# Kernel optimization log

Hardware: AMD Instinct MI355X
Metric: run time of the kernel (lower is better)

The kernel has to match this reference:

```python
import jax, jax.numpy as jnp
import numpy as np
from jax import lax

EPS = 1e-5

def binarize(x):
    # sign() forward, straight-through (identity) backward, like BinarizeConv2d's .data trick
    return x + lax.stop_gradient(jnp.sign(x) - x)

def conv_nchw(x, w, stride, pad):
    return lax.conv_general_dilated(
        x, w, window_strides=(stride, stride), padding=((pad, pad), (pad, pad)),
        dimension_numbers=('NCHW', 'OIHW', 'NCHW'))

def batchnorm_train(x, gamma, beta):
    # training-mode BN: per-channel batch mean / biased variance over (N,H,W)
    mean = jnp.mean(x, axis=(0, 2, 3), keepdims=True)
    var = jnp.mean((x - mean) ** 2, axis=(0, 2, 3), keepdims=True)
    xhat = (x - mean) * lax.rsqrt(var + EPS)
    return xhat * gamma[None, :, None, None] + beta[None, :, None, None]

def hardtanh(x):
    return jnp.clip(x, -1.0, 1.0)

def setup_inputs() -> dict:
    key = jax.random.key(0)
    ks = jax.random.split(key, 7)
    N, Cin, Cout, H, W = 32, 64, 64, 128, 128
    x = jax.random.normal(ks[0], (N, Cin, H, W), dtype=jnp.float32)
    w1 = jax.random.normal(ks[1], (Cout, Cin, 3, 3), dtype=jnp.float32) * 0.05
    w2 = jax.random.normal(ks[2], (Cout, Cout, 3, 3), dtype=jnp.float32) * 0.05
    g1 = jnp.ones((Cout,), dtype=jnp.float32)
    b1 = jnp.zeros((Cout,), dtype=jnp.float32)
    g2 = jnp.ones((Cout,), dtype=jnp.float32)
    b2 = jnp.zeros((Cout,), dtype=jnp.float32)
    return {"x": x, "w1": w1, "g1": g1, "b1": b1, "w2": w2, "g2": g2, "b2": b2}

def reference(x, w1, g1, b1, w2, g2, b2):
    # conv1: binarized input (C=64 != 3) and binarized weights
    out = conv_nchw(binarize(x), binarize(w1), stride=1, pad=1)
    out = hardtanh(batchnorm_train(out, g1, b1))
    # conv2: 3x3, stride 1 (stride==1 branch)
    out = conv_nchw(binarize(out), binarize(w2), stride=1, pad=1)
    out = batchnorm_train(out, g2, b2)
    # identity shortcut (stride==1 and in_planes==planes)
    out = out + x
    return hardtanh(out)
```

## Files before the change

kernel.cpp:

```cpp
#include <hip/hip_runtime.h>
#include <stdint.h>

typedef unsigned long long u64;
typedef unsigned int u32;

#define Nn 32
#define Cc 64
#define Hh 128
#define Ww 128
#define HPAD 130
#define WPAD 130
#define NHW_TOT (Nn*Hh*Ww)
#define NBIN 8

__device__ __forceinline__ float2 compute_ab(const u64* __restrict__ sum, const u64* __restrict__ sq,
        const float* __restrict__ g, const float* __restrict__ bet, int c) {
    long long Sv = 0, Qv = 0;
    #pragma unroll
    for (int b = 0; b < NBIN; ++b) {
        Sv += (long long)sum[b * 64 + c];
        Qv += (long long)sq[b * 64 + c];
    }
    double mean = (double)Sv / (double)NHW_TOT;
    double var = (double)Qv / (double)NHW_TOT - mean * mean;
    double invstd = 1.0 / sqrt(var + 1e-5);
    double a = (double)g[c] * invstd;
    double b_ = (double)bet[c] - a * mean;
    return make_float2((float)a, (float)b_);
}

__global__ __launch_bounds__(256) void pack_x4_kernel(const float* __restrict__ x,
                                                      u64* __restrict__ xpad) {
    int t = blockIdx.x * 256 + threadIdx.x;
    int P = t * 4;
    int row = P >> 7, w0 = P & 127;
    int n = row >> 7, h = row & 127;
    const float4* xp4 = (const float4*)(x + ((size_t)n * Cc * Hh + h) * Ww + w0);
    u32 lo0 = 0, lo1 = 0, lo2 = 0, lo3 = 0, hi0 = 0, hi1 = 0, hi2 = 0, hi3 = 0;
    #pragma unroll 8
    for (int c = 0; c < 32; ++c) {
        float4 v = xp4[c * (Hh * Ww / 4)];
        lo0 |= (__float_as_uint(v.x) >> 31) << c;
        lo1 |= (__float_as_uint(v.y) >> 31) << c;
        lo2 |= (__float_as_uint(v.z) >> 31) << c;
        lo3 |= (__float_as_uint(v.w) >> 31) << c;
    }
    #pragma unroll 8
    for (int c = 32; c < 64; ++c) {
        float4 v = xp4[c * (Hh * Ww / 4)];
        hi0 |= (__float_as_uint(v.x) >> 31) << (c - 32);
        hi1 |= (__float_as_uint(v.y) >> 31) << (c - 32);
        hi2 |= (__float_as_uint(v.z) >> 31) << (c - 32);
        hi3 |= (__float_as_uint(v.w) >> 31) << (c - 32);
    }
    u64* dst = xpad + ((size_t)n * HPAD + h + 1) * WPAD + w0 + 1;
    dst[0] = ((u64)hi0 << 32) | lo0;
    dst[1] = ((u64)hi1 << 32) | lo1;
    dst[2] = ((u64)hi2 << 32) | lo2;
    dst[3] = ((u64)hi3 << 32) | lo3;
}

__global__ __launch_bounds__(576) void pack_w_kernel(
        const float* __restrict__ w1, const float* __restrict__ w2,
        u64* __restrict__ w1b, u64* __restrict__ w2b) {
    int t = threadIdx.x;
    const float* src = blockIdx.x ? w2 : w1;
    u64* db = blockIdx.x ? w2b : w1b;
    int co = t / 9, tap = t - co * 9;
    const float* p = src + (size_t)co * 576 + tap;
    u32 lo = 0, hi = 0;
    #pragma unroll
    for (int ci = 0; ci < 32; ++ci)
        lo |= (__float_as_uint(p[ci * 9]) >> 31) << ci;
    #pragma unroll
    for (int ci = 32; ci < 64; ++ci)
        hi |= (__float_as_uint(p[ci * 9]) >> 31) << (ci - 32);
    db[t] = ((u64)hi << 32) | lo;
}

__device__ __forceinline__ void conv4(const u64* __restrict__ L0, const u64* __restrict__ L1,
                                      const u64* __restrict__ L2, int w,
                                      const u64 W[9], int corrMid, int v[4]) {
    u64 a[6], b[6], c[6];
    #pragma unroll
    for (int j = 0; j < 6; ++j) { a[j] = L0[w + j]; b[j] = L1[w + j]; c[j] = L2[w + j]; }
    #pragma unroll
    for (int px = 0; px < 4; ++px) {
        int p0 = __popcll(a[px] ^ W[0]) + __popcll(a[px + 1] ^ W[1]) + __popcll(a[px + 2] ^ W[2]);
        int p1 = __popcll(b[px] ^ W[3]) + __popcll(b[px + 1] ^ W[4]) + __popcll(b[px + 2] ^ W[5]);
        int p2 = __popcll(c[px] ^ W[6]) + __popcll(c[px + 1] ^ W[7]) + __popcll(c[px + 2] ^ W[8]);
        v[px] = 576 - 2 * (p0 + p1 + p2) - corrMid;
    }
}

struct LaneCtx {
    u64 W[9];
    int corrMid, corrW0, corrW127;
    int n, h;
};

__device__ __forceinline__ void lane_setup(LaneCtx& C, const u64* __restrict__ wb,
                                           int lane, int blk, int wv) {
    C.n = blk >> 5;
    int hb = (blk & 31) << 2;
    C.h = hb + wv;
    #pragma unroll
    for (int t = 0; t < 9; ++t) C.W[t] = wb[lane * 9 + t];
    int wc[9];
    #pragma unroll
    for (int t = 0; t < 9; ++t) wc[t] = 64 - 2 * __popcll(C.W[t]);
    int tT = wc[0] + wc[1] + wc[2], tB = wc[6] + wc[7] + wc[8];
    int tL = wc[0] + wc[3] + wc[6], tR = wc[2] + wc[5] + wc[8];
    bool fT = (C.h == 0), fB = (C.h == 127);
    C.corrMid  = (fT ? tT : 0) + (fB ? tB : 0);
    C.corrW0   = tL - (fT ? wc[0] : 0) - (fB ? wc[6] : 0);
    C.corrW127 = tR - (fT ? wc[2] : 0) - (fB ? wc[8] : 0);
}

template<bool SPILL>
__global__ __launch_bounds__(256) void conv_statsT(const u64* __restrict__ inpad,
        const u64* __restrict__ wb, u64* __restrict__ gsum, u64* __restrict__ gsq,
        short* __restrict__ v16) {
    __shared__ u64 win[6 * 130];
    int tid = threadIdx.x;
    int lane = tid & 63;
    int wv = __builtin_amdgcn_readfirstlane(tid >> 6);
    int blk = blockIdx.x;
    int n = blk >> 5, hb = (blk & 31) << 2;
    const u64* src = inpad + ((size_t)n * HPAD + hb) * WPAD;
    for (int i = tid; i < 780; i += 256) win[i] = src[i];
    LaneCtx C;
    lane_setup(C, wb, lane, blk, wv);
    __syncthreads();
    const u64* L0 = &win[wv * 130];
    const u64* L1 = L0 + 130;
    const u64* L2 = L0 + 260;
    short* vrow = SPILL ? (v16 + ((size_t)(C.n * Hh + C.h) * Ww) * 64 + lane) : nullptr;
    int s = 0, q = 0;
    for (int w = 0; w < 128; w += 4) {
        int v[4];
        conv4(L0, L1, L2, w, C.W, C.corrMid, v);
        if (w == 0)   v[0] -= C.corrW0;
        if (w == 124) v[3] -= C.corrW127;
        #pragma unroll
        for (int px = 0; px < 4; ++px) {
            s += v[px];
            q += __mul24(v[px], v[px]);
            if (SPILL) vrow[(size_t)(w + px) * 64] = (short)v[px];
        }
    }
    __syncthreads();
    int* r32 = (int*)win;
    r32[wv * 64 + lane] = s;
    r32[256 + wv * 64 + lane] = q;
    __syncthreads();
    if (wv == 0) {
        int S = r32[lane] + r32[64 + lane] + r32[128 + lane] + r32[192 + lane];
        int Q = r32[256 + lane] + r32[320 + lane] + r32[384 + lane] + r32[448 + lane];
        int bin = blk & (NBIN - 1);
        atomicAdd(&gsum[bin * 64 + lane], (u64)(long long)S);
        atomicAdd(&gsq[bin * 64 + lane], (u64)(long long)Q);
    }
}

__global__ __launch_bounds__(256) void signpack_v(const short* __restrict__ v16,
        const u64* __restrict__ sum, const u64* __restrict__ sq,
        const float* __restrict__ g, const float* __restrict__ bet,
        u64* __restrict__ ypad) {
    int tid = threadIdx.x;
    int lane = tid & 63;
    int wv = tid >> 6;
    int grow = blockIdx.x * 4 + wv;
    int n = grow >> 7, h = grow & 127;
    float2 ab = compute_ab(sum, sq, g, bet, lane);
    const short* vr = v16 + (size_t)grow * (Ww * 64) + lane;
    u64* drow = ypad + ((size_t)n * HPAD + h + 1) * WPAD + 1;
    for (int base = 0; base < 128; base += 64) {
        u64 myw = 0;
        #pragma unroll 8
        for (int px = 0; px < 64; ++px) {
            float tv = fmaf((float)vr[(size_t)(base + px) * 64], ab.x, ab.y);
            u64 bal = __ballot(tv < 0.0f);
            if (lane == px) myw = bal;
        }
        drow[base + lane] = myw;
    }
}

__global__ __launch_bounds__(256) void signpack_rc(const u64* __restrict__ inpad,
        const u64* __restrict__ wb, const u64* __restrict__ sum, const u64* __restrict__ sq,
        const float* __restrict__ g, const float* __restrict__ bet,
        u64* __restrict__ outpad) {
    __shared__ u64 win[6 * 130];
    int tid = threadIdx.x;
    int lane = tid & 63;
    int wv = __builtin_amdgcn_readfirstlane(tid >> 6);
    int blk = blockIdx.x;
    int n = blk >> 5, hb = (blk & 31) << 2;
    const u64* src = inpad + ((size_t)n * HPAD + hb) * WPAD;
    for (int i = tid; i < 780; i += 256) win[i] = src[i];
    LaneCtx C;
    lane_setup(C, wb, lane, blk, wv);
    float2 ab = compute_ab(sum, sq, g, bet, lane);
    __syncthreads();
    const u64* L0 = &win[wv * 130];
    const u64* L1 = L0 + 130;
    const u64* L2 = L0 + 260;
    u64* drow = outpad + ((size_t)C.n * HPAD + C.h + 1) * WPAD + 1;
    for (int w = 0; w < 128; w += 4) {
        int v[4];
        conv4(L0, L1, L2, w, C.W, C.corrMid, v);
        if (w == 0)   v[0] -= C.corrW0;
        if (w == 124) v[3] -= C.corrW127;
        u64 wd[4];
        #pragma unroll
        for (int px = 0; px < 4; ++px) {
            float t = fmaf((float)v[px], ab.x, ab.y);
            wd[px] = __ballot(t < 0.0f);
        }
        if (lane == 0) {
            drow[w] = wd[0]; drow[w + 1] = wd[1]; drow[w + 2] = wd[2]; drow[w + 3] = wd[3];
        }
    }
}

__global__ __launch_bounds__(256) void final4_kernel(const u64* __restrict__ inpad,
        const u64* __restrict__ wb, const u64* __restrict__ sum, const u64* __restrict__ sq,
        const float* __restrict__ g, const float* __restrict__ bet,
        const float* __restrict__ x, float* __restrict__ out) {
    __shared__ u64 win[6 * 130];
    __shared__ float tile[4][64 * 33];
    int tid = threadIdx.x;
    int lane = tid & 63;
    int wv = __builtin_amdgcn_readfirstlane(tid >> 6);
    int blk = blockIdx.x;
    int n = blk >> 5, hb = (blk & 31) << 2;
    const u64* src = inpad + ((size_t)n * HPAD + hb) * WPAD;
    for (int i = tid; i < 780; i += 256) win[i] = src[i];
    LaneCtx C;
    lane_setup(C, wb, lane, blk, wv);
    float2 ab = compute_ab(sum, sq, g, bet, lane);
    float aa = ab.x, bb = ab.y;
    __syncthreads();
    const u64* L0 = &win[wv * 130];
    const u64* L1 = L0 + 130;
    const u64* L2 = L0 + 260;
    float* T = tile[wv];
    int p4 = lane & 7;
    int cosub = lane >> 3;
    size_t base_nch = ((size_t)C.n * Cc * Hh + C.h) * Ww;
    for (int w = 0; w < 128; w += 4) {
        int v[4];
        conv4(L0, L1, L2, w, C.W, C.corrMid, v);
        if (w == 0)   v[0] -= C.corrW0;
        if (w == 124) v[3] -= C.corrW127;
        #pragma unroll
        for (int px = 0; px < 4; ++px) {
            float t = fmaf((float)v[px], aa, bb);
            T[lane * 33 + ((w + px) & 31)] = t;
        }
        if ((w & 31) == 28) {
            int w0 = w & ~31;
            #pragma unroll 8
            for (int st = 0; st < 8; ++st) {
                int co = st * 8 + cosub;
                size_t idx = base_nch + (size_t)co * (Hh * Ww) + w0 + p4 * 4;
                float4 xv = *(const float4*)(x + idx);
                float y0 = T[co * 33 + p4 * 4 + 0] + xv.x;
                float y1 = T[co * 33 + p4 * 4 + 1] + xv.y;
                float y2 = T[co * 33 + p4 * 4 + 2] + xv.z;
                float y3 = T[co * 33 + p4 * 4 + 3] + xv.w;
                float4 yv;
                yv.x = fminf(1.0f, fmaxf(-1.0f, y0));
                yv.y = fminf(1.0f, fmaxf(-1.0f, y1));
                yv.z = fminf(1.0f, fmaxf(-1.0f, y2));
                yv.w = fminf(1.0f, fmaxf(-1.0f, y3));
                *(float4*)(out + idx) = yv;
            }
        }
    }
}

extern "C" void kernel_launch(void* const* d_in, const int* in_sizes, int n_in,
                              void* d_out, int out_size, void* d_ws, size_t ws_size,
                              hipStream_t stream) {
    const float* x  = (const float*)d_in[0];
    const float* w1 = (const float*)d_in[1];
    const float* g1 = (const float*)d_in[2];
    const float* b1 = (const float*)d_in[3];
    const float* w2 = (const float*)d_in[4];
    const float* g2 = (const float*)d_in[5];
    const float* b2 = (const float*)d_in[6];
    float* out = (float*)d_out;
    char* ws = (char*)d_ws;

    constexpr size_t SZ_PAD   = (size_t)Nn * HPAD * WPAD * sizeof(u64);
    constexpr size_t OFF_YPAD = SZ_PAD;
    constexpr size_t OFF_STAT = 2 * SZ_PAD;
    constexpr size_t SZ_STAT  = (size_t)NBIN * 64 * 8;
    constexpr size_t OFF_W1B  = OFF_STAT + 4 * SZ_STAT;
    constexpr size_t OFF_W2B  = OFF_W1B + 576 * 8;
    constexpr size_t OFF_V16  = OFF_W2B + 576 * 8;
    constexpr size_t SZ_V16   = (size_t)Nn * Hh * Ww * 64 * 2;
    constexpr size_t WS_SMALL = OFF_V16;
    constexpr size_t WS_FULL  = OFF_V16 + SZ_V16;

    if (ws_size < WS_SMALL) return;
    bool spill = (ws_size >= WS_FULL);

    u64* xpad = (u64*)(ws);
    u64* ypad = (u64*)(ws + OFF_YPAD);
    u64* gsum1 = (u64*)(ws + OFF_STAT);
    u64* gsq1  = (u64*)(ws + OFF_STAT + SZ_STAT);
    u64* gsum2 = (u64*)(ws + OFF_STAT + 2 * SZ_STAT);
    u64* gsq2  = (u64*)(ws + OFF_STAT + 3 * SZ_STAT);
    u64* w1b  = (u64*)(ws + OFF_W1B);
    u64* w2b  = (u64*)(ws + OFF_W2B);
    short* v16 = (short*)(ws + OFF_V16);

    hipMemsetAsync(ws, 0, 2 * SZ_PAD + 4 * SZ_STAT, stream);

    pack_x4_kernel<<<512, 256, 0, stream>>>(x, xpad);
    pack_w_kernel<<<2, 576, 0, stream>>>(w1, w2, w1b, w2b);
    if (spill) {
        conv_statsT<true><<<1024, 256, 0, stream>>>(xpad, w1b, gsum1, gsq1, v16);
        signpack_v<<<1024, 256, 0, stream>>>(v16, gsum1, gsq1, g1, b1, ypad);
    } else {
        conv_statsT<false><<<1024, 256, 0, stream>>>(xpad, w1b, gsum1, gsq1, nullptr);
        signpack_rc<<<1024, 256, 0, stream>>>(xpad, w1b, gsum1, gsq1, g1, b1, ypad);
    }
    conv_statsT<false><<<1024, 256, 0, stream>>>(ypad, w2b, gsum2, gsq2, nullptr);
    final4_kernel<<<1024, 256, 0, stream>>>(ypad, w2b, gsum2, gsq2, g2, b2, x, out);
}
```

Before: 228.1 us.

## Split conv blocks into half-row tiles with more blocks and smaller LDS

The conv-stats and final kernels are retiled from one 256-thread block per four full rows to 128-thread blocks covering two rows and half the width. This gives a 4096-block grid with a smaller LDS window. The final kernel now stages raw conv values as shorts in LDS, computes the BN affine per channel from a shared table, and applies it while reading back. The stat bins double to 16 to spread out atomic contention, and signpack_v now gives each wave half a row. The goal is more parallelism and occupancy, at the cost of redundant halo loads and more per-block setup such as loading weights.

```diff
diff --git a/kernel.cpp b/kernel.cpp
--- a/kernel.cpp
+++ b/kernel.cpp
@@ -11,7 +11,7 @@
 #define HPAD 130
 #define WPAD 130
 #define NHW_TOT (Nn*Hh*Ww)
-#define NBIN 8
+#define NBIN 16
 
 __device__ __forceinline__ float2 compute_ab(const u64* __restrict__ sum, const u64* __restrict__ sq,
         const float* __restrict__ g, const float* __restrict__ bet, int c) {
@@ -96,14 +96,10 @@
 struct LaneCtx {
     u64 W[9];
     int corrMid, corrW0, corrW127;
-    int n, h;
 };
 
 __device__ __forceinline__ void lane_setup(LaneCtx& C, const u64* __restrict__ wb,
-                                           int lane, int blk, int wv) {
-    C.n = blk >> 5;
-    int hb = (blk & 31) << 2;
-    C.h = hb + wv;
+                                           int lane, int h) {
     #pragma unroll
     for (int t = 0; t < 9; ++t) C.W[t] = wb[lane * 9 + t];
     int wc[9];
@@ -111,37 +107,44 @@
     for (int t = 0; t < 9; ++t) wc[t] = 64 - 2 * __popcll(C.W[t]);
     int tT = wc[0] + wc[1] + wc[2], tB = wc[6] + wc[7] + wc[8];
     int tL = wc[0] + wc[3] + wc[6], tR = wc[2] + wc[5] + wc[8];
-    bool fT = (C.h == 0), fB = (C.h == 127);
+    bool fT = (h == 0), fB = (h == 127);
     C.corrMid  = (fT ? tT : 0) + (fB ? tB : 0);
     C.corrW0   = tL - (fT ? wc[0] : 0) - (fB ? wc[6] : 0);
     C.corrW127 = tR - (fT ? wc[2] : 0) - (fB ? wc[8] : 0);
 }
 
 template<bool SPILL>
-__global__ __launch_bounds__(256) void conv_statsT(const u64* __restrict__ inpad,
+__global__ __launch_bounds__(128) void conv_statsT(const u64* __restrict__ inpad,
         const u64* __restrict__ wb, u64* __restrict__ gsum, u64* __restrict__ gsq,
         short* __restrict__ v16) {
-    __shared__ u64 win[6 * 130];
+    __shared__ u64 win[4 * 68];
+    __shared__ int r32[256];
     int tid = threadIdx.x;
     int lane = tid & 63;
     int wv = __builtin_amdgcn_readfirstlane(tid >> 6);
     int blk = blockIdx.x;
-    int n = blk >> 5, hb = (blk & 31) << 2;
-    const u64* src = inpad + ((size_t)n * HPAD + hb) * WPAD;
-    for (int i = tid; i < 780; i += 256) win[i] = src[i];
+    int half = blk & 1;
+    int hp = (blk >> 1) & 63;
+    int n = blk >> 7;
+    int h = hp * 2 + wv;
+    const u64* src = inpad + ((size_t)n * HPAD + hp * 2) * WPAD + half * 64;
+    for (int i = tid; i < 264; i += 128) {
+        int r = i / 66, c = i - r * 66;
+        win[r * 68 + c] = src[(size_t)r * WPAD + c];
+    }
     LaneCtx C;
-    lane_setup(C, wb, lane, blk, wv);
-    __syncthreads();
-    const u64* L0 = &win[wv * 130];
-    const u64* L1 = L0 + 130;
-    const u64* L2 = L0 + 260;
-    short* vrow = SPILL ? (v16 + ((size_t)(C.n * Hh + C.h) * Ww) * 64 + lane) : nullptr;
+    lane_setup(C, wb, lane, h);
+    __syncthreads();
+    const u64* L0 = &win[wv * 68];
+    const u64* L1 = L0 + 68;
+    const u64* L2 = L0 + 136;
+    short* vrow = SPILL ? (v16 + (((size_t)(n * Hh + h) * Ww) + half * 64) * 64 + lane) : nullptr;
     int s = 0, q = 0;
-    for (int w = 0; w < 128; w += 4) {
+    for (int w = 0; w < 64; w += 4) {
         int v[4];
         conv4(L0, L1, L2, w, C.W, C.corrMid, v);
-        if (w == 0)   v[0] -= C.corrW0;
-        if (w == 124) v[3] -= C.corrW127;
+        if (half == 0 && w == 0)  v[0] -= C.corrW0;
+        if (half == 1 && w == 60) v[3] -= C.corrW127;
         #pragma unroll
         for (int px = 0; px < 4; ++px) {
             s += v[px];
@@ -150,13 +153,12 @@
         }
     }
     __syncthreads();
-    int* r32 = (int*)win;
     r32[wv * 64 + lane] = s;
-    r32[256 + wv * 64 + lane] = q;
+    r32[128 + wv * 64 + lane] = q;
     __syncthreads();
     if (wv == 0) {
-        int S = r32[lane] + r32[64 + lane] + r32[128 + lane] + r32[192 + lane];
-        int Q = r32[256 + lane] + r32[320 + lane] + r32[384 + lane] + r32[448 + lane];
+        int S = r32[lane] + r32[64 + lane];
+        int Q = r32[128 + lane] + r32[192 + lane];
         int bin = blk & (NBIN - 1);
         atomicAdd(&gsum[bin * 64 + lane], (u64)(long long)S);
         atomicAdd(&gsq[bin * 64 + lane], (u64)(long long)Q);
@@ -170,21 +172,20 @@
     int tid = threadIdx.x;
     int lane = tid & 63;
     int wv = tid >> 6;
-    int grow = blockIdx.x * 4 + wv;
+    int grow = blockIdx.x * 2 + (wv >> 1);
+    int base = (wv & 1) * 64;
     int n = grow >> 7, h = grow & 127;
     float2 ab = compute_ab(sum, sq, g, bet, lane);
-    const short* vr = v16 + (size_t)grow * (Ww * 64) + lane;
+    const short* vr = v16 + ((size_t)grow * Ww + base) * 64;
     u64* drow = ypad + ((size_t)n * HPAD + h + 1) * WPAD + 1;
-    for (int base = 0; base < 128; base += 64) {
-        u64 myw = 0;
-        #pragma unroll 8
-        for (int px = 0; px < 64; ++px) {
-            float tv = fmaf((float)vr[(size_t)(base + px) * 64], ab.x, ab.y);
-            u64 bal = __ballot(tv < 0.0f);
-            if (lane == px) myw = bal;
-        }
-        drow[base + lane] = myw;
-    }
+    u64 myw = 0;
+    #pragma unroll 8
+    for (int px = 0; px < 64; ++px) {
+        float tv = fmaf((float)vr[(size_t)px * 64 + lane], ab.x, ab.y);
+        u64 bal = __ballot(tv < 0.0f);
+        if (lane == px) myw = bal;
+    }
+    drow[base + lane] = myw;
 }
 
 __global__ __launch_bounds__(256) void signpack_rc(const u64* __restrict__ inpad,
@@ -197,16 +198,17 @@
     int wv = __builtin_amdgcn_readfirstlane(tid >> 6);
     int blk = blockIdx.x;
     int n = blk >> 5, hb = (blk & 31) << 2;
+    int h = hb + wv;
     const u64* src = inpad + ((size_t)n * HPAD + hb) * WPAD;
     for (int i = tid; i < 780; i += 256) win[i] = src[i];
     LaneCtx C;
-    lane_setup(C, wb, lane, blk, wv);
+    lane_setup(C, wb, lane, h);
     float2 ab = compute_ab(sum, sq, g, bet, lane);
     __syncthreads();
     const u64* L0 = &win[wv * 130];
     const u64* L1 = L0 + 130;
     const u64* L2 = L0 + 260;
-    u64* drow = outpad + ((size_t)C.n * HPAD + C.h + 1) * WPAD + 1;
+    u64* drow = outpad + ((size_t)n * HPAD + h + 1) * WPAD + 1;
     for (int w = 0; w < 128; w += 4) {
         int v[4];
         conv4(L0, L1, L2, w, C.W, C.corrMid, v);
@@ -224,57 +226,59 @@
     }
 }
 
-__global__ __launch_bounds__(256) void final4_kernel(const u64* __restrict__ inpad,
+__global__ __launch_bounds__(128) void final5_kernel(const u64* __restrict__ inpad,
         const u64* __restrict__ wb, const u64* __restrict__ sum, const u64* __restrict__ sq,
         const float* __restrict__ g, const float* __restrict__ bet,
         const float* __restrict__ x, float* __restrict__ out) {
-    __shared__ u64 win[6 * 130];
-    __shared__ float tile[4][64 * 33];
+    __shared__ u64 win[4 * 68];
+    __shared__ short T[2][64 * 36];
+    __shared__ float2 absh[64];
     int tid = threadIdx.x;
     int lane = tid & 63;
     int wv = __builtin_amdgcn_readfirstlane(tid >> 6);
     int blk = blockIdx.x;
-    int n = blk >> 5, hb = (blk & 31) << 2;
-    const u64* src = inpad + ((size_t)n * HPAD + hb) * WPAD;
-    for (int i = tid; i < 780; i += 256) win[i] = src[i];
+    int half = blk & 1;
+    int hp = (blk >> 1) & 63;
+    int n = blk >> 7;
+    int h = hp * 2 + wv;
+    const u64* src = inpad + ((size_t)n * HPAD + hp * 2) * WPAD + half * 64;
+    for (int i = tid; i < 264; i += 128) {
+        int r = i / 66, c = i - r * 66;
+        win[r * 68 + c] = src[(size_t)r * WPAD + c];
+    }
     LaneCtx C;
-    lane_setup(C, wb, lane, blk, wv);
-    float2 ab = compute_ab(sum, sq, g, bet, lane);
-    float aa = ab.x, bb = ab.y;
-    __syncthreads();
-    const u64* L0 = &win[wv * 130];
-    const u64* L1 = L0 + 130;
-    const u64* L2 = L0 + 260;
-    float* T = tile[wv];
+    lane_setup(C, wb, lane, h);
+    if (tid < 64) absh[tid] = compute_ab(sum, sq, g, bet, tid);
+    __syncthreads();
+    const u64* L0 = &win[wv * 68];
+    const u64* L1 = L0 + 68;
+    const u64* L2 = L0 + 136;
+    short* Tw = T[wv];
     int p4 = lane & 7;
     int cosub = lane >> 3;
-    size_t base_nch = ((size_t)C.n * Cc * Hh + C.h) * Ww;
-    for (int w = 0; w < 128; w += 4) {
+    size_t base_nch = ((size_t)n * Cc * Hh + h) * Ww;
+    for (int w = 0; w < 64; w += 4) {
         int v[4];
         conv4(L0, L1, L2, w, C.W, C.corrMid, v);
-        if (w == 0)   v[0] -= C.corrW0;
-        if (w == 124) v[3] -= C.corrW127;
-        #pragma unroll
-        for (int px = 0; px < 4; ++px) {
-            float t = fmaf((float)v[px], aa, bb);
-            T[lane * 33 + ((w + px) & 31)] = t;
-        }
+        if (half == 0 && w == 0)  v[0] -= C.corrW0;
+        if (half == 1 && w == 60) v[3] -= C.corrW127;
+        short4 sv;
+        sv.x = (short)v[0]; sv.y = (short)v[1]; sv.z = (short)v[2]; sv.w = (short)v[3];
+        *(short4*)&Tw[lane * 36 + (w & 31)] = sv;
         if ((w & 31) == 28) {
-            int w0 = w & ~31;
+            int w0g = half * 64 + (w & ~31);
             #pragma unroll 8
             for (int st = 0; st < 8; ++st) {
                 int co = st * 8 + cosub;
-                size_t idx = base_nch + (size_t)co * (Hh * Ww) + w0 + p4 * 4;
+                short4 tv = *(const short4*)&Tw[co * 36 + p4 * 4];
+                float2 cab = absh[co];
+                size_t idx = base_nch + (size_t)co * (Hh * Ww) + w0g + p4 * 4;
                 float4 xv = *(const float4*)(x + idx);
-                float y0 = T[co * 33 + p4 * 4 + 0] + xv.x;
-                float y1 = T[co * 33 + p4 * 4 + 1] + xv.y;
-                float y2 = T[co * 33 + p4 * 4 + 2] + xv.z;
-                float y3 = T[co * 33 + p4 * 4 + 3] + xv.w;
                 float4 yv;
-                yv.x = fminf(1.0f, fmaxf(-1.0f, y0));
-                yv.y = fminf(1.0f, fmaxf(-1.0f, y1));
-                yv.z = fminf(1.0f, fmaxf(-1.0f, y2));
-                yv.w = fminf(1.0f, fmaxf(-1.0f, y3));
+                yv.x = fminf(1.0f, fmaxf(-1.0f, fmaf((float)tv.x, cab.x, cab.y) + xv.x));
+                yv.y = fminf(1.0f, fmaxf(-1.0f, fmaf((float)tv.y, cab.x, cab.y) + xv.y));
+                yv.z = fminf(1.0f, fmaxf(-1.0f, fmaf((float)tv.z, cab.x, cab.y) + xv.z));
+                yv.w = fminf(1.0f, fmaxf(-1.0f, fmaf((float)tv.w, cab.x, cab.y) + xv.w));
                 *(float4*)(out + idx) = yv;
             }
         }
@@ -323,12 +327,12 @@
     pack_x4_kernel<<<512, 256, 0, stream>>>(x, xpad);
     pack_w_kernel<<<2, 576, 0, stream>>>(w1, w2, w1b, w2b);
     if (spill) {
-        conv_statsT<true><<<1024, 256, 0, stream>>>(xpad, w1b, gsum1, gsq1, v16);
-        signpack_v<<<1024, 256, 0, stream>>>(v16, gsum1, gsq1, g1, b1, ypad);
+        conv_statsT<true><<<4096, 128, 0, stream>>>(xpad, w1b, gsum1, gsq1, v16);
+        signpack_v<<<2048, 256, 0, stream>>>(v16, gsum1, gsq1, g1, b1, ypad);
     } else {
-        conv_statsT<false><<<1024, 256, 0, stream>>>(xpad, w1b, gsum1, gsq1, nullptr);
+        conv_statsT<false><<<4096, 128, 0, stream>>>(xpad, w1b, gsum1, gsq1, nullptr);
         signpack_rc<<<1024, 256, 0, stream>>>(xpad, w1b, gsum1, gsq1, g1, b1, ypad);
     }
-    conv_statsT<false><<<1024, 256, 0, stream>>>(ypad, w2b, gsum2, gsq2, nullptr);
-    final4_kernel<<<1024, 256, 0, stream>>>(ypad, w2b, gsum2, gsq2, g2, b2, x, out);
-}
+    conv_statsT<false><<<4096, 128, 0, stream>>>(ypad, w2b, gsum2, gsq2, nullptr);
+    final5_kernel<<<4096, 128, 0, stream>>>(ypad, w2b, gsum2, gsq2, g2, b2, x, out);
+}
```

Result: faster. 221.7 us (-2.8%).
